# Kernel optimization log

Hardware: AMD Instinct MI355X
Metric: run time of the kernel (lower is better)

## Reference

```python
import jax, jax.numpy as jnp
import numpy as np
from jax import lax

EPS = 1e-5
DN_CONV = ('NCDHW', 'OIDHW', 'NCDHW')
DN_TCONV = ('NCDHW', 'DHWIO', 'NCDHW')


def conv3(x, w, s):
    # 3x3x3 conv, padding 1 (dense analogue of sparse conv on the voxel grid)
    return lax.conv_general_dilated(x, w, (s, s, s), [(1, 1)] * 3, dimension_numbers=DN_CONV)


def tconv3(x, w, s):
    # 3x3x3 transposed conv; stride 2 doubles spatial size, stride 1 keeps it
    return lax.conv_transpose(x, w, (s, s, s), 'SAME', dimension_numbers=DN_TCONV)


def bn_relu(x, g, b):
    # BatchNorm over (N,D,H,W) per channel, training-mode batch stats, then ReLU
    m = jnp.mean(x, (0, 2, 3, 4), keepdims=True)
    v = jnp.var(x, (0, 2, 3, 4), keepdims=True)
    y = (x - m) * lax.rsqrt(v + EPS) * g[None, :, None, None, None] + b[None, :, None, None, None]
    return jax.nn.relu(y)


def setup_inputs() -> dict:
    key = jax.random.key(0)
    ks = jax.random.split(key, 8)
    W = lambda k, shape: jax.random.normal(k, shape, dtype=jnp.float32) * 0.05
    inp = {
        'x': jax.random.normal(ks[0], (2, 16, 64, 64, 64), dtype=jnp.float32),
        # encoder convs (OIDHW)
        'w0': W(ks[1], (32, 16, 3, 3, 3)), 'g0': jnp.ones((32,)), 'b0': jnp.zeros((32,)),
        'w1': W(ks[2], (64, 32, 3, 3, 3)), 'g1': jnp.ones((64,)), 'b1': jnp.zeros((64,)),
        'w2': W(ks[3], (128, 64, 3, 3, 3)), 'g2': jnp.ones((128,)), 'b2': jnp.zeros((128,)),
        # reconstruction decoder transposed convs (DHWIO)
        'wt2r': W(ks[4], (3, 3, 3, 128, 64)), 'g2r': jnp.ones((64,)), 'b2r': jnp.zeros((64,)),
        'wt1r': W(ks[5], (3, 3, 3, 64, 32)), 'g1r': jnp.ones((32,)), 'b1r': jnp.zeros((32,)),
        'wt0r': W(jax.random.fold_in(key, 10), (3, 3, 3, 32, 16)),
        # classification decoder transposed convs
        'wt2c': W(ks[6], (3, 3, 3, 128, 64)), 'g2c': jnp.ones((64,)), 'b2c': jnp.zeros((64,)),
        'wt1c': W(ks[7], (3, 3, 3, 128, 64)), 'g1c': jnp.ones((64,)), 'b1c': jnp.zeros((64,)),
        'wt0c': W(jax.random.fold_in(key, 11), (3, 3, 3, 96, 2)),
    }
    return inp


def reference(x, w0, g0, b0, w1, g1, b1, w2, g2, b2,
              wt2r, g2r, b2r, wt1r, g1r, b1r, wt0r,
              wt2c, g2c, b2c, wt1c, g1c, b1c, wt0c):
    # encoder
    s1 = bn_relu(conv3(x, w0, 1), g0, b0)      # [N,32,64,64,64]
    s2 = bn_relu(conv3(s1, w1, 2), g1, b1)     # [N,64,32,32,32]
    s4 = bn_relu(conv3(s2, w2, 2), g2, b2)     # [N,128,16,16,16]
    # reconstruction head
    rec = bn_relu(tconv3(s4, wt2r, 2), g2r, b2r)  # [N,64,32,...]
    # classification head with skip concats
    cl = bn_relu(tconv3(s4, wt2c, 2), g2c, b2c)   # [N,64,32,...]
    cl = jnp.concatenate([cl, s2], axis=1)        # [N,128,32,...]
    rec = bn_relu(tconv3(rec, wt1r, 2), g1r, b1r)  # [N,32,64,...]
    cl = bn_relu(tconv3(cl, wt1c, 2), g1c, b1c)    # [N,64,64,...]
    cl = jnp.concatenate([cl, s1], axis=1)         # [N,96,64,...]
    rec = tconv3(rec, wt0r, 1)                     # [N,16,64,...]
    cl = tconv3(cl, wt0c, 1)                       # [N,2,64,...]
    return (cl, rec)
```

## Files before the change

kernel.cpp:

```cpp
#include <hip/hip_runtime.h>
#include <hip/hip_bf16.h>


using bf16 = __hip_bfloat16;
using ushort4v = __attribute__((ext_vector_type(4))) unsigned short;
using ushort8  = __attribute__((ext_vector_type(8))) unsigned short;
using short8   = __attribute__((ext_vector_type(8))) short;
using f32x4    = __attribute__((ext_vector_type(4))) float;
using float4v  = __attribute__((ext_vector_type(4))) float;

#define TPB 256

static inline int cdiv_l(long a, int b){ return (int)((a + b - 1) / b); }

__device__ __forceinline__ float b2f(unsigned short u){
  union { unsigned int i; float f; } v; v.i = ((unsigned int)u) << 16; return v.f;
}
__device__ __forceinline__ unsigned short f2b(float f){
  union { bf16 h; unsigned short u; } v; v.h = __float2bfloat16(f); return v.u;
}
__device__ __forceinline__ ushort8 bnApply8(ushort8 v, const float* sc, const float* sh, int c){
  float4v s0 = *(const float4v*)(sc + c), s1v = *(const float4v*)(sc + c + 4);
  float4v h0 = *(const float4v*)(sh + c), h1v = *(const float4v*)(sh + c + 4);
  ushort8 r;
#pragma unroll
  for (int j = 0; j < 4; ++j){ float y = b2f(v[j]) * s0[j] + h0[j]; r[j] = f2b(y > 0.f ? y : 0.f); }
#pragma unroll
  for (int j = 0; j < 4; ++j){ float y = b2f(v[j+4]) * s1v[j] + h1v[j]; r[j+4] = f2b(y > 0.f ? y : 0.f); }
  return r;
}

__global__ void rp_all(const float* __restrict__ w0, const float* __restrict__ w1,
                       const float* __restrict__ w2, const float* __restrict__ wt2r,
                       const float* __restrict__ wt2c, const float* __restrict__ wt1r,
                       const float* __restrict__ wt1c, const float* __restrict__ wt0r,
                       const float* __restrict__ wt0c,
                       unsigned short* __restrict__ wb0p, unsigned short* __restrict__ wb1,
                       unsigned short* __restrict__ wb2, unsigned short* __restrict__ wb2r,
                       unsigned short* __restrict__ wb2c, unsigned short* __restrict__ wb1r,
                       unsigned short* __restrict__ wb1c, unsigned short* __restrict__ wbrec,
                       unsigned short* __restrict__ wbcl){
  int idx = blockIdx.x * TPB + threadIdx.x;
  auto enc = [](const float* w, unsigned short* d, int i, int Cin, int Cout){
    int ci = i % Cin; int t = i / Cin; int co = t % Cout; int tap = t / Cout;
    d[i] = f2b(w[((long)co * Cin + ci) * 27 + tap]);
  };
  auto dec = [](const float* w, unsigned short* d, int i, int Cin, int Cout, int CIP, int COP){
    int ci = i % CIP; int t = i / CIP; int co = t % COP; int tap = t / COP;
    float v = (ci < Cin && co < Cout) ? w[((long)tap * Cin + ci) * Cout + co] : 0.f;
    d[i] = f2b(v);
  };
  if (idx < 14336) {
    int i = idx;
    int k = i & 31; int t = i >> 5; int co = t & 31; int pp = t >> 5;
    int tap = pp * 2 + (k >> 4); int ci = k & 15;
    float v = (tap < 27) ? w0[((long)co * 16 + ci) * 27 + tap] : 0.f;
    wb0p[i] = f2b(v);
  }
  else if (idx <   69632) enc(w1,  wb1,  idx - 14336,  32, 64);
  else if (idx <  290816) enc(w2,  wb2,  idx - 69632,  64, 128);
  else if (idx <  512000) dec(wt2r, wb2r, idx - 290816, 128, 64, 128, 64);
  else if (idx <  733184) dec(wt2c, wb2c, idx - 512000, 128, 64, 128, 64);
  else if (idx <  788480) dec(wt1r, wb1r, idx - 733184,  64, 32,  64, 32);
  else if (idx < 1009664) dec(wt1c, wb1c, idx - 788480, 128, 64, 128, 64);
  else if (idx < 1023488) dec(wt0r, wbrec, idx - 1009664, 32, 16,  32, 16);
  else if (idx < 1064960) dec(wt0c, wbcl, idx - 1023488, 96,  2,  96, 16);
}

__global__ void xpose_k(const float* __restrict__ x, unsigned short* __restrict__ xt){
  __shared__ float l[16][257];
  int t = threadIdx.x;
  long p0 = (long)blockIdx.x * 256;
  int n = (int)(p0 >> 18);
  long off = p0 & 262143;
  const float* xb = x + ((long)n * 16) * 262144 + off;
#pragma unroll
  for (int c = 0; c < 16; ++c) l[c][t] = xb[(long)c * 262144 + t];
  __syncthreads();
  ushort8 u0, u1;
#pragma unroll
  for (int k = 0; k < 8; ++k){ u0[k] = f2b(l[k][t]); u1[k] = f2b(l[k + 8][t]); }
  unsigned short* o = xt + (p0 + t) * 16;
  *(ushort8*)o = u0; *(ushort8*)(o + 8) = u1;
}

template <int CO_TILES, bool STATS>
__global__ __launch_bounds__(TPB, 2) void tconv_quad(
    const unsigned short* __restrict__ inA, int CA,
    const unsigned short* __restrict__ inB, int CB,
    const float* __restrict__ scA, const float* __restrict__ shA,
    const unsigned short* __restrict__ wb,
    unsigned short* __restrict__ out,
    float* __restrict__ part2, int NB,
    int N, int Cout, int COP, int CIP, int G) {
  __shared__ unsigned short xs[2][4 * 432 * 8];
  const int tid = threadIdx.x, wv = tid >> 6, l = tid & 63, l15 = l & 15, lg = l >> 4;
  int ntW = G >> 4, ntH = G >> 2, ntD = G >> 2;
  int bx = blockIdx.x;
  const int blkLin = blockIdx.x * 4 + blockIdx.z;
  int w0 = (bx % ntW) << 4; bx /= ntW;
  int h0 = (bx % ntH) << 2; bx /= ntH;
  int d0 = (bx % ntD) << 2; int n = bx / ntD;
  const int co0 = blockIdx.y * (16 * CO_TILES);
  const int quad = blockIdx.z;
  const int pd = (quad >> 1) & 1, ph = quad & 1;
  const long spin = (long)G * G * G;

  int nkd, kd_[2], dd_[2], nkh, kh_[2], dh_[2];
  if (pd){ nkd=1; kd_[0]=1; dd_[0]=0; } else { nkd=2; kd_[0]=0; dd_[0]=-1; kd_[1]=2; dd_[1]=0; }
  if (ph){ nkh=1; kh_[0]=1; dh_[0]=0; } else { nkh=2; kh_[0]=0; dh_[0]=-1; kh_[1]=2; dh_[1]=0; }

  f32x4 acc[CO_TILES][4][2];
#pragma unroll
  for (int ct = 0; ct < CO_TILES; ++ct)
#pragma unroll
    for (int j = 0; j < 4; ++j)
#pragma unroll
      for (int p = 0; p < 2; ++p) acc[ct][j][p] = (f32x4){0.f, 0.f, 0.f, 0.f};

  auto stage = [&](int ch, int buf) {
    int c0 = ch << 5;
    const unsigned short* src; int Cs, cl_; bool useBN;
    if (c0 < CA){ src = inA; Cs = CA; cl_ = c0; useBN = (scA != nullptr); }
    else        { src = inB; Cs = CB; cl_ = c0 - CA; useBN = false; }
    const unsigned short* sb = src + (long)n * Cs * spin;
    unsigned short* xb = &xs[buf][0];
    for (int idx = tid; idx < 4 * 425; idx += TPB) {
      int q = idx / 425, pt = idx - q * 425;
      int zw = pt % 17; int zt = pt / 17; int zh = zt % 5; int zd = zt / 5;
      int gd = d0 + zd - 1, gh = h0 + zh - 1, gw = w0 + zw - 1;
      ushort8 v = (ushort8){0,0,0,0,0,0,0,0};
      if ((unsigned)gd < (unsigned)G && (unsigned)gh < (unsigned)G && (unsigned)gw < (unsigned)G) {
        v = *(const ushort8*)(sb + (((long)gd * G + gh) * G + gw) * Cs + cl_ + q * 8);
        if (useBN) v = bnApply8(v, scA, shA, cl_ + q * 8);
      }
      *(ushort8*)(xb + (q * 432 + pt) * 8) = v;
    }
  };

  const int nch = CIP >> 5;
  stage(0, 0);
  __syncthreads();
#pragma unroll 1
  for (int ch = 0; ch < nch; ++ch) {
    int cur = ch & 1;
    int c0 = ch << 5;
    if (ch + 1 < nch) stage(ch + 1, cur ^ 1);
    const unsigned short* xr = &xs[cur][0];
#pragma unroll 1
    for (int a = 0; a < nkd; ++a) {
      int zd = wv + 1 + dd_[a];
#pragma unroll 1
      for (int b = 0; b < nkh; ++b) {
        int tapb = (kd_[a] * 3 + kh_[b]) * 3;
        const unsigned short* ap = wb + ((long)tapb * COP + co0 + l15) * CIP + c0 + lg * 8;
        long tstride = (long)COP * CIP;
        short8 Ak0[CO_TILES], Ak1[CO_TILES], Ak2[CO_TILES];
#pragma unroll
        for (int ct = 0; ct < CO_TILES; ++ct) {
          Ak0[ct] = *(const short8*)(ap + ct * 16 * CIP);
          Ak1[ct] = *(const short8*)(ap + tstride + ct * 16 * CIP);
          Ak2[ct] = *(const short8*)(ap + 2 * tstride + ct * 16 * CIP);
        }
        int zh0 = 1 + dh_[b];
#pragma unroll
        for (int j = 0; j < 4; ++j) {
          int basept = (zd * 5 + (j + zh0)) * 17 + l15;
          short8 Bm = *(const short8*)(xr + (lg * 432 + basept) * 8);
          short8 B0 = *(const short8*)(xr + (lg * 432 + basept + 1) * 8);
#pragma unroll
          for (int ct = 0; ct < CO_TILES; ++ct) {
            acc[ct][j][0] = __builtin_amdgcn_mfma_f32_16x16x32_bf16(Ak0[ct], Bm, acc[ct][j][0], 0, 0, 0);
            acc[ct][j][0] = __builtin_amdgcn_mfma_f32_16x16x32_bf16(Ak2[ct], B0, acc[ct][j][0], 0, 0, 0);
            acc[ct][j][1] = __builtin_amdgcn_mfma_f32_16x16x32_bf16(Ak1[ct], B0, acc[ct][j][1], 0, 0, 0);
          }
        }
      }
    }
    __syncthreads();
  }

  int Gout = 2 * G; long spo = (long)Gout * Gout * Gout;
  int od = 2 * (d0 + wv) + pd;
#pragma unroll
  for (int j = 0; j < 4; ++j) {
    int oh = 2 * (h0 + j) + ph;
#pragma unroll
    for (int p = 0; p < 2; ++p) {
      int ow = 2 * (w0 + l15) + p;
      long pt = ((long)od * Gout + oh) * Gout + ow;
#pragma unroll
      for (int ct = 0; ct < CO_TILES; ++ct) {
        ushort4v pk;
#pragma unroll
        for (int r = 0; r < 4; ++r) pk[r] = f2b(acc[ct][j][p][r]);
        *(ushort4v*)(out + ((long)n * spo + pt) * Cout + co0 + ct * 16 + lg * 4) = pk;
      }
    }
  }

  if constexpr (STATS) {
    __shared__ float redS[4][CO_TILES][4][4];
    __shared__ float redQ[4][CO_TILES][4][4];
#pragma unroll
    for (int ct = 0; ct < CO_TILES; ++ct)
#pragma unroll
      for (int r = 0; r < 4; ++r) {
        float s = 0.f, q = 0.f;
#pragma unroll
        for (int j = 0; j < 4; ++j)
#pragma unroll
          for (int p = 0; p < 2; ++p) { float a = acc[ct][j][p][r]; s += a; q += a * a; }
#pragma unroll
        for (int m = 1; m < 16; m <<= 1) { s += __shfl_xor(s, m); q += __shfl_xor(q, m); }
        if (l15 == 0) { redS[wv][ct][lg][r] = s; redQ[wv][ct][lg][r] = q; }
      }
    __syncthreads();
    if (tid < CO_TILES * 16) {
      int ct = tid >> 4, lg2 = (tid >> 2) & 3, r = tid & 3;
      float s = 0.f, q = 0.f;
#pragma unroll
      for (int w2 = 0; w2 < 4; ++w2) { s += redS[w2][ct][lg2][r]; q += redQ[w2][ct][lg2][r]; }
      int c = co0 + ct * 16 + lg2 * 4 + r;
      long slot = (long)c * NB + blkLin;
      part2[slot * 2] = s; part2[slot * 2 + 1] = q;
    }
  }
}

__global__ __launch_bounds__(TPB) void tconv_dual(
    const unsigned short* __restrict__ in, int CI,
    const float* __restrict__ scA, const float* __restrict__ shA,
    const unsigned short* __restrict__ wbA, const unsigned short* __restrict__ wbB,
    unsigned short* __restrict__ outA, unsigned short* __restrict__ outB,
    float* __restrict__ p2A, float* __restrict__ p2B, int NB,
    int N, int Cout, int COP, int CIP, int G) {
  const int CT = 2;
  __shared__ unsigned short xs[4 * 432 * 8];
  const int tid = threadIdx.x, wv = tid >> 6, l = tid & 63, l15 = l & 15, lg = l >> 4;
  int ntW = G >> 4, ntH = G >> 2, ntD = G >> 2;
  int bx = blockIdx.x;
  const int blkLin = blockIdx.x * 4 + blockIdx.z;
  int w0 = (bx % ntW) << 4; bx /= ntW;
  int h0 = (bx % ntH) << 2; bx /= ntH;
  int d0 = (bx % ntD) << 2; int n = bx / ntD;
  const int co0 = blockIdx.y * (16 * CT);
  const int quad = blockIdx.z;
  const int pd = (quad >> 1) & 1, ph = quad & 1;
  const long spin = (long)G * G * G;

  int nkd, kd_[2], dd_[2], nkh, kh_[2], dh_[2];
  if (pd){ nkd=1; kd_[0]=1; dd_[0]=0; } else { nkd=2; kd_[0]=0; dd_[0]=-1; kd_[1]=2; dd_[1]=0; }
  if (ph){ nkh=1; kh_[0]=1; dh_[0]=0; } else { nkh=2; kh_[0]=0; dh_[0]=-1; kh_[1]=2; dh_[1]=0; }

  f32x4 acc[2][CT][4][2];
#pragma unroll
  for (int h = 0; h < 2; ++h)
#pragma unroll
    for (int ct = 0; ct < CT; ++ct)
#pragma unroll
      for (int j = 0; j < 4; ++j)
#pragma unroll
        for (int p = 0; p < 2; ++p) acc[h][ct][j][p] = (f32x4){0.f, 0.f, 0.f, 0.f};

  const int nch = CIP >> 5;
#pragma unroll 1
  for (int ch = 0; ch < nch; ++ch) {
    int c0 = ch << 5;
    const unsigned short* sb = in + (long)n * CI * spin;
    __syncthreads();
    for (int idx = tid; idx < 4 * 425; idx += TPB) {
      int q = idx / 425, pt = idx - q * 425;
      int zw = pt % 17; int zt = pt / 17; int zh = zt % 5; int zd = zt / 5;
      int gd = d0 + zd - 1, gh = h0 + zh - 1, gw = w0 + zw - 1;
      ushort8 v = (ushort8){0,0,0,0,0,0,0,0};
      if ((unsigned)gd < (unsigned)G && (unsigned)gh < (unsigned)G && (unsigned)gw < (unsigned)G) {
        v = *(const ushort8*)(sb + (((long)gd * G + gh) * G + gw) * CI + c0 + q * 8);
        v = bnApply8(v, scA, shA, c0 + q * 8);
      }
      *(ushort8*)(xs + (q * 432 + pt) * 8) = v;
    }
    __syncthreads();
#pragma unroll 1
    for (int a = 0; a < nkd; ++a) {
      int zd = wv + 1 + dd_[a];
#pragma unroll 1
      for (int b = 0; b < nkh; ++b) {
        int tapb = (kd_[a] * 3 + kh_[b]) * 3;
        long tstride = (long)COP * CIP;
        long abase = ((long)tapb * COP + co0 + l15) * CIP + c0 + lg * 8;
        int zh0 = 1 + dh_[b];
#pragma unroll
        for (int h = 0; h < 2; ++h) {
          const unsigned short* ap = (h == 0 ? wbA : wbB) + abase;
          short8 Ak0[CT], Ak1[CT], Ak2[CT];
#pragma unroll
          for (int ct = 0; ct < CT; ++ct) {
            Ak0[ct] = *(const short8*)(ap + ct * 16 * CIP);
            Ak1[ct] = *(const short8*)(ap + tstride + ct * 16 * CIP);
            Ak2[ct] = *(const short8*)(ap + 2 * tstride + ct * 16 * CIP);
          }
#pragma unroll
          for (int j = 0; j < 4; ++j) {
            int basept = (zd * 5 + (j + zh0)) * 17 + l15;
            short8 Bm = *(const short8*)(xs + (lg * 432 + basept) * 8);
            short8 B0 = *(const short8*)(xs + (lg * 432 + basept + 1) * 8);
#pragma unroll
            for (int ct = 0; ct < CT; ++ct) {
              acc[h][ct][j][0] = __builtin_amdgcn_mfma_f32_16x16x32_bf16(Ak0[ct], Bm, acc[h][ct][j][0], 0, 0, 0);
              acc[h][ct][j][0] = __builtin_amdgcn_mfma_f32_16x16x32_bf16(Ak2[ct], B0, acc[h][ct][j][0], 0, 0, 0);
              acc[h][ct][j][1] = __builtin_amdgcn_mfma_f32_16x16x32_bf16(Ak1[ct], B0, acc[h][ct][j][1], 0, 0, 0);
            }
          }
        }
      }
    }
  }

  int Gout = 2 * G; long spo = (long)Gout * Gout * Gout;
  int od = 2 * (d0 + wv) + pd;
#pragma unroll
  for (int j = 0; j < 4; ++j) {
    int oh = 2 * (h0 + j) + ph;
#pragma unroll
    for (int p = 0; p < 2; ++p) {
      int ow = 2 * (w0 + l15) + p;
      long pt = ((long)od * Gout + oh) * Gout + ow;
#pragma unroll
      for (int h = 0; h < 2; ++h) {
        unsigned short* o = h == 0 ? outA : outB;
#pragma unroll
        for (int ct = 0; ct < CT; ++ct) {
          ushort4v pk;
#pragma unroll
          for (int r = 0; r < 4; ++r) pk[r] = f2b(acc[h][ct][j][p][r]);
          *(ushort4v*)(o + ((long)n * spo + pt) * Cout + co0 + ct * 16 + lg * 4) = pk;
        }
      }
    }
  }

  __shared__ float redS[4][CT][4][4];
  __shared__ float redQ[4][CT][4][4];
#pragma unroll 1
  for (int h = 0; h < 2; ++h) {
    __syncthreads();
#pragma unroll
    for (int ct = 0; ct < CT; ++ct)
#pragma unroll
      for (int r = 0; r < 4; ++r) {
        float s = 0.f, q = 0.f;
#pragma unroll
        for (int j = 0; j < 4; ++j)
#pragma unroll
          for (int p = 0; p < 2; ++p) { float a = acc[h][ct][j][p][r]; s += a; q += a * a; }
#pragma unroll
        for (int m = 1; m < 16; m <<= 1) { s += __shfl_xor(s, m); q += __shfl_xor(q, m); }
        if (l15 == 0) { redS[wv][ct][lg][r] = s; redQ[wv][ct][lg][r] = q; }
      }
    __syncthreads();
    if (tid < CT * 16) {
      int ct = tid >> 4, lg2 = (tid >> 2) & 3, r = tid & 3;
      float s = 0.f, q = 0.f;
#pragma unroll
      for (int w2 = 0; w2 < 4; ++w2) { s += redS[w2][ct][lg2][r]; q += redQ[w2][ct][lg2][r]; }
      int c = co0 + ct * 16 + lg2 * 4 + r;
      long slot = (long)c * NB + blkLin;
      float* p2 = h == 0 ? p2A : p2B;
      p2[slot * 2] = s; p2[slot * 2 + 1] = q;
    }
  }
}

template <int VARIANT, int CO_TILES, bool PAIRED, bool FOUT, bool STATS>
__global__ __launch_bounds__(TPB) void mconv(
    const unsigned short* __restrict__ inA, int CA,
    const unsigned short* __restrict__ inB, int CB,
    const float* __restrict__ scA, const float* __restrict__ shA,
    const unsigned short* __restrict__ wb,
    void* __restrict__ outv,
    float* __restrict__ part2, int NB,
    int N, int Cout, int COP, int CIP, int G) {
  const int tid = threadIdx.x, wv = tid >> 6, l = tid & 63, l15 = l & 15, lg = l >> 4;
  int bx = blockIdx.x;
  const int blkLin = blockIdx.x;
  int w0, h0, d0, n;
  int wvd = wv & 1, jh = wv >> 1, jbase = jh * 4;
  if constexpr (VARIANT == 0) {
    int ntW = G >> 4, ntH = G >> 3, ntD = G >> 1;
    w0 = (bx % ntW) << 4; bx /= ntW;
    h0 = (bx % ntH) << 3; bx /= ntH;
    d0 = (bx % ntD) << 1; n = bx / ntD;
  } else {
    int ntW = G >> 4, ntH = G >> 2, ntD = G >> 2;
    w0 = (bx % ntW) << 4; bx /= ntW;
    h0 = (bx % ntH) << 2; bx /= ntH;
    d0 = (bx % ntD) << 2; n = bx / ntD;
  }
  const int co0 = blockIdx.y * (16 * CO_TILES);
  const int Gin = (VARIANT == 2) ? 2 * G : G;
  const long spin = (long)Gin * Gin * Gin;

  f32x4 acc[CO_TILES][4];
#pragma unroll
  for (int ct = 0; ct < CO_TILES; ++ct)
#pragma unroll
    for (int j = 0; j < 4; ++j) acc[ct][j] = (f32x4){0.f, 0.f, 0.f, 0.f};

  if constexpr (PAIRED) {
    __shared__ unsigned short xs[2 * 728 * 8];
    const unsigned short* src = inA + (long)n * 16 * spin;
    for (int idx = tid; idx < 2 * 720; idx += TPB) {
      int q = idx / 720, pt = idx - q * 720;
      int zw = pt % 18; int zt = pt / 18; int zh = zt % 10; int zd = zt / 10;
      int gd = d0 + zd - 1, gh = h0 + zh - 1, gw = w0 + zw - 1;
      ushort8 v = (ushort8){0,0,0,0,0,0,0,0};
      if ((unsigned)gd < (unsigned)G && (unsigned)gh < (unsigned)G && (unsigned)gw < (unsigned)G)
        v = *(const ushort8*)(src + (((long)gd * G + gh) * G + gw) * 16 + q * 8);
      *(ushort8*)(xs + (q * 728 + pt) * 8) = v;
    }
    __syncthreads();
#pragma unroll 1
    for (int pp = 0; pp < 14; ++pp) {
      short8 A0 = *(const short8*)(wb + ((pp * 32 + l15) * 32) + lg * 8);
      short8 A1 = *(const short8*)(wb + ((pp * 32 + 16 + l15) * 32) + lg * 8);
      int t0 = 2 * pp + (lg >> 1); if (t0 > 26) t0 = 26;
      int dd = t0 / 9 - 1, dh = (t0 / 3) % 3 - 1, dw = t0 % 3 - 1;
      int q = lg & 1;
      int zd = wvd + 1 + dd;
      int base = (q * 728 + (zd * 10 + (1 + dh + jbase)) * 18 + 1 + l15 + dw) * 8;
#pragma unroll
      for (int j = 0; j < 4; ++j) {
        short8 B = *(const short8*)(xs + base + j * (18 * 8));
        acc[0][j] = __builtin_amdgcn_mfma_f32_16x16x32_bf16(A0, B, acc[0][j], 0, 0, 0);
        if (CO_TILES == 2)
          acc[1][j] = __builtin_amdgcn_mfma_f32_16x16x32_bf16(A1, B, acc[1][j], 0, 0, 0);
      }
    }
  } else if constexpr (VARIANT == 0) {
    __shared__ unsigned short xs[4 * 728 * 8];
    const int nch = CIP >> 5;
#pragma unroll 1
    for (int ch = 0; ch < nch; ++ch) {
      int c0 = ch << 5;
      const unsigned short* src; int Cs, cl_; bool useBN;
      if (c0 < CA){ src = inA; Cs = CA; cl_ = c0; useBN = (scA != nullptr); }
      else        { src = inB; Cs = CB; cl_ = c0 - CA; useBN = false; }
      const unsigned short* sb = src + (long)n * Cs * spin;
      __syncthreads();
      for (int idx = tid; idx < 4 * 720; idx += TPB) {
        int q = idx / 720, pt = idx - q * 720;
        int zw = pt % 18; int zt = pt / 18; int zh = zt % 10; int zd = zt / 10;
        int gd = d0 + zd - 1, gh = h0 + zh - 1, gw = w0 + zw - 1;
        ushort8 v = (ushort8){0,0,0,0,0,0,0,0};
        if ((unsigned)gd < (unsigned)G && (unsigned)gh < (unsigned)G && (unsigned)gw < (unsigned)G) {
          v = *(const ushort8*)(sb + (((long)gd * G + gh) * G + gw) * Cs + cl_ + q * 8);
          if (useBN) v = bnApply8(v, scA, shA, cl_ + q * 8);
        }
        *(ushort8*)(xs + (q * 728 + pt) * 8) = v;
      }
      __syncthreads();
#pragma unroll 1
      for (int a = 0; a < 3; ++a) {
        int zd = wvd + a;
        short8 A0[3][3], A1[3][3];
#pragma unroll
        for (int b = 0; b < 3; ++b)
#pragma unroll
          for (int c = 0; c < 3; ++c) {
            int tap = (a * 3 + b) * 3 + c;
            const unsigned short* ap = wb + ((long)tap * COP + co0 + l15) * CIP + c0 + lg * 8;
            A0[b][c] = *(const short8*)ap;
            if (CO_TILES == 2) A1[b][c] = *(const short8*)(ap + 16 * CIP);
          }
#pragma unroll
        for (int sl = 0; sl < 6; ++sl) {
          int sg = jbase + sl;
          int rb = (lg * 728 + (zd * 10 + sg) * 18 + l15) * 8;
          short8 B0 = *(const short8*)(xs + rb);
          short8 B1 = *(const short8*)(xs + rb + 8);
          short8 B2 = *(const short8*)(xs + rb + 16);
#pragma unroll
          for (int b = 0; b < 3; ++b) {
            int j = sl - b;
            if (j >= 0 && j < 4) {
              acc[0][j] = __builtin_amdgcn_mfma_f32_16x16x32_bf16(A0[b][0], B0, acc[0][j], 0, 0, 0);
              acc[0][j] = __builtin_amdgcn_mfma_f32_16x16x32_bf16(A0[b][1], B1, acc[0][j], 0, 0, 0);
              acc[0][j] = __builtin_amdgcn_mfma_f32_16x16x32_bf16(A0[b][2], B2, acc[0][j], 0, 0, 0);
              if (CO_TILES == 2) {
                acc[1][j] = __builtin_amdgcn_mfma_f32_16x16x32_bf16(A1[b][0], B0, acc[1][j], 0, 0, 0);
                acc[1][j] = __builtin_amdgcn_mfma_f32_16x16x32_bf16(A1[b][1], B1, acc[1][j], 0, 0, 0);
                acc[1][j] = __builtin_amdgcn_mfma_f32_16x16x32_bf16(A1[b][2], B2, acc[1][j], 0, 0, 0);
              }
            }
          }
        }
      }
    }
  } else {
    const int nch = CIP >> 5;
#pragma unroll 1
    for (int ch = 0; ch < nch; ++ch) {
      int c0 = ch << 5;
      const unsigned short* src; int Cs, cl_;
      if (c0 < CA){ src = inA; Cs = CA; cl_ = c0; } else { src = inB; Cs = CB; cl_ = c0 - CA; }
      const unsigned short* sb = src + (long)n * Cs * spin;
#pragma unroll 1
      for (int a = 0; a < 3; ++a) {
        int gd = 2 * (d0 + wv) + a - 1;
        bool vd = (unsigned)gd < (unsigned)Gin;
#pragma unroll 1
        for (int b = 0; b < 3; ++b) {
#pragma unroll
          for (int c = 0; c < 3; ++c) {
            int tap = (a * 3 + b) * 3 + c;
            const unsigned short* ap = wb + ((long)tap * COP + co0 + l15) * CIP + c0 + lg * 8;
            short8 A0 = *(const short8*)ap;
            short8 A1;
            if (CO_TILES == 2) A1 = *(const short8*)(ap + 16 * CIP);
            int gw = 2 * (w0 + l15) + c - 1;
            bool vdw = vd && ((unsigned)gw < (unsigned)Gin);
#pragma unroll
            for (int j = 0; j < 4; ++j) {
              int gh = 2 * (h0 + j) + b - 1;
              short8 B = (short8){0,0,0,0,0,0,0,0};
              if (vdw && (unsigned)gh < (unsigned)Gin)
                B = *(const short8*)(sb + (((long)gd * Gin + gh) * Gin + gw) * Cs + cl_ + lg * 8);
              acc[0][j] = __builtin_amdgcn_mfma_f32_16x16x32_bf16(A0, B, acc[0][j], 0, 0, 0);
              if (CO_TILES == 2)
                acc[1][j] = __builtin_amdgcn_mfma_f32_16x16x32_bf16(A1, B, acc[1][j], 0, 0, 0);
            }
          }
        }
      }
    }
  }

  const long spo = (long)G * G * G;
#pragma unroll
  for (int j = 0; j < 4; ++j) {
    long pt;
    if constexpr (VARIANT == 0)
      pt = ((long)(d0 + wvd) * G + (h0 + jbase + j)) * G + (w0 + l15);
    else
      pt = ((long)(d0 + wv) * G + (h0 + j)) * G + (w0 + l15);
    if constexpr (!FOUT) {
      unsigned short* outp = (unsigned short*)outv;
#pragma unroll
      for (int ct = 0; ct < CO_TILES; ++ct) {
        ushort4v pk;
#pragma unroll
        for (int r = 0; r < 4; ++r) pk[r] = f2b(acc[ct][j][r]);
        *(ushort4v*)(outp + ((long)n * spo + pt) * Cout + co0 + ct * 16 + lg * 4) = pk;
      }
    } else {
      float* outp = (float*)outv;
#pragma unroll
      for (int ct = 0; ct < CO_TILES; ++ct)
#pragma unroll
        for (int r = 0; r < 4; ++r) {
          int co = co0 + ct * 16 + lg * 4 + r;
          if (co < Cout) outp[((long)(n * Cout + co)) * spo + pt] = acc[ct][j][r];
        }
    }
  }

  if constexpr (STATS) {
    __shared__ float redS[4][CO_TILES][4][4];
    __shared__ float redQ[4][CO_TILES][4][4];
#pragma unroll
    for (int ct = 0; ct < CO_TILES; ++ct)
#pragma unroll
      for (int r = 0; r < 4; ++r) {
        float s = 0.f, q = 0.f;
#pragma unroll
        for (int j = 0; j < 4; ++j) { float a = acc[ct][j][r]; s += a; q += a * a; }
#pragma unroll
        for (int m = 1; m < 16; m <<= 1) { s += __shfl_xor(s, m); q += __shfl_xor(q, m); }
        if (l15 == 0) { redS[wv][ct][lg][r] = s; redQ[wv][ct][lg][r] = q; }
      }
    __syncthreads();
    if (tid < CO_TILES * 16) {
      int ct = tid >> 4, lg2 = (tid >> 2) & 3, r = tid & 3;
      float s = 0.f, q = 0.f;
#pragma unroll
      for (int w2 = 0; w2 < 4; ++w2) { s += redS[w2][ct][lg2][r]; q += redQ[w2][ct][lg2][r]; }
      int c = co0 + ct * 16 + lg2 * 4 + r;
      long slot = (long)c * NB + blkLin;
      part2[slot * 2] = s; part2[slot * 2 + 1] = q;
    }
  }
}

__global__ void bn_stats2b(const float* __restrict__ part2, const float* __restrict__ g,
                           const float* __restrict__ b, float* __restrict__ sc,
                           float* __restrict__ sh, int NB, float inv_cnt){
  int c = blockIdx.x, tid = threadIdx.x;
  float s = 0.f, q = 0.f;
  for (int i = tid; i < NB; i += TPB) {
    s += part2[((long)c * NB + i) * 2];
    q += part2[((long)c * NB + i) * 2 + 1];
  }
  __shared__ float ss[TPB], qq[TPB];
  ss[tid] = s; qq[tid] = q;
  __syncthreads();
  for (int off = TPB / 2; off > 0; off >>= 1) {
    if (tid < off) { ss[tid] += ss[tid + off]; qq[tid] += qq[tid + off]; }
    __syncthreads();
  }
  if (tid == 0) {
    float m = ss[0] * inv_cnt, v = qq[0] * inv_cnt - m * m;
    float rs = rsqrtf(v + 1e-5f) * g[c];
    sc[c] = rs;
    sh[c] = b[c] - m * rs;
  }
}

__global__ void bn_relu_cl(unsigned short* __restrict__ x, const float* __restrict__ sc,
                           const float* __restrict__ sh, int C, long tot8){
  long i8 = (long)blockIdx.x * TPB + threadIdx.x;
  if (i8 >= tot8) return;
  long e = i8 * 8;
  int c0 = (int)(e & (C - 1));
  ushort8 v = *(ushort8*)(x + e);
  *(ushort8*)(x + e) = bnApply8(v, sc, sh, c0);
}

extern "C" void kernel_launch(void* const* d_in, const int* in_sizes, int n_in,
                              void* d_out, int out_size, void* d_ws, size_t ws_size,
                              hipStream_t stream) {
  const float* x    = (const float*)d_in[0];
  const float* w0   = (const float*)d_in[1];
  const float* g0   = (const float*)d_in[2];
  const float* b0   = (const float*)d_in[3];
  const float* w1   = (const float*)d_in[4];
  const float* g1   = (const float*)d_in[5];
  const float* b1   = (const float*)d_in[6];
  const float* w2   = (const float*)d_in[7];
  const float* g2   = (const float*)d_in[8];
  const float* b2   = (const float*)d_in[9];
  const float* wt2r = (const float*)d_in[10];
  const float* g2r  = (const float*)d_in[11];
  const float* b2r  = (const float*)d_in[12];
  const float* wt1r = (const float*)d_in[13];
  const float* g1r  = (const float*)d_in[14];
  const float* b1r  = (const float*)d_in[15];
  const float* wt0r = (const float*)d_in[16];
  const float* wt2c = (const float*)d_in[17];
  const float* g2c  = (const float*)d_in[18];
  const float* b2c  = (const float*)d_in[19];
  const float* wt1c = (const float*)d_in[20];
  const float* g1c  = (const float*)d_in[21];
  const float* b1c  = (const float*)d_in[22];
  const float* wt0c = (const float*)d_in[23];

  const int N = 2;
  const long sp64 = 262144, sp32 = 32768, sp16 = 4096;

  unsigned short* W = (unsigned short*)d_ws;
  unsigned short* s1   = W;
  unsigned short* s2   = s1  + 16777216;
  unsigned short* s4   = s2  + 4194304;
  unsigned short* r32  = s4  + 1048576;
  unsigned short* c32  = r32 + 4194304;
  unsigned short* r64  = c32 + 4194304;
  unsigned short* xt   = r64;
  unsigned short* c64  = r64 + 16777216;
  unsigned short* wb0p = c64 + 33554432;
  unsigned short* wb1  = wb0p + 14336;
  unsigned short* wb2  = wb1  + 55296;
  unsigned short* wb2r = wb2  + 221184;
  unsigned short* wb2c = wb2r + 221184;
  unsigned short* wb1r = wb2c + 221184;
  unsigned short* wb1c = wb1r + 55296;
  unsigned short* wbrec= wb1c + 221184;
  unsigned short* wbcl = wbrec+ 13824;
  float* part2  = (float*)(wbcl + 41472);
  float* part2b = part2 + 131072;
  float* bsc  = part2b + 16384;
  float* bsh  = bsc + 128;
  float* sc_s4  = bsh  + 128; float* sh_s4  = sc_s4  + 128;
  float* sc_r32 = sh_s4 + 128; float* sh_r32 = sc_r32 + 128;
  float* sc_c32 = sh_r32+ 128; float* sh_c32 = sc_c32 + 128;
  float* sc_r64 = sh_c32+ 128; float* sh_r64 = sc_r64 + 128;
  float* sc_c64 = sh_r64+ 128; float* sh_c64 = sc_c64 + 128;

  float* out_cl  = (float*)d_out;
  float* out_rec = (float*)d_out + 2L * 2 * sp64;

  rp_all<<<cdiv_l(1064960, TPB), TPB, 0, stream>>>(
      w0, w1, w2, wt2r, wt2c, wt1r, wt1c, wt0r, wt0c,
      wb0p, wb1, wb2, wb2r, wb2c, wb1r, wb1c, wbrec, wbcl);
  xpose_k<<<2048, TPB, 0, stream>>>(x, xt);

  auto gx0 = [&](int G){ return (unsigned)(N * (G >> 1) * (G >> 3) * (G >> 4)); };
  auto gx  = [&](int G){ return (unsigned)(N * (G >> 2) * (G >> 2) * (G >> 4)); };

  mconv<0, 2, true, false, true><<<dim3(gx0(64), 1), TPB, 0, stream>>>(
      xt, 16, nullptr, 0, nullptr, nullptr, wb0p, s1, part2, (int)gx0(64), N, 32, 32, 32, 64);
  bn_stats2b<<<32, TPB, 0, stream>>>(part2, g0, b0, bsc, bsh, (int)gx0(64), 1.f / (float)(2 * sp64));
  bn_relu_cl<<<cdiv_l(2 * sp64 * 32 / 8, TPB), TPB, 0, stream>>>(s1, bsc, bsh, 32, 2 * sp64 * 32 / 8);

  mconv<2, 2, false, false, true><<<dim3(gx(32), 2), TPB, 0, stream>>>(
      s1, 32, nullptr, 0, nullptr, nullptr, wb1, s2, part2, (int)gx(32), N, 64, 64, 32, 32);
  bn_stats2b<<<64, TPB, 0, stream>>>(part2, g1, b1, bsc, bsh, (int)gx(32), 1.f / (float)(2 * sp32));
  bn_relu_cl<<<cdiv_l(2 * sp32 * 64 / 8, TPB), TPB, 0, stream>>>(s2, bsc, bsh, 64, 2 * sp32 * 64 / 8);

  mconv<2, 1, false, false, true><<<dim3(gx(16), 8), TPB, 0, stream>>>(
      s2, 64, nullptr, 0, nullptr, nullptr, wb2, s4, part2, (int)gx(16), N, 128, 128, 64, 16);
  bn_stats2b<<<128, TPB, 0, stream>>>(part2, g2, b2, sc_s4, sh_s4, (int)gx(16), 1.f / (float)(2 * sp16));

  tconv_dual<<<dim3(gx(16), 2, 4), TPB, 0, stream>>>(
      s4, 128, sc_s4, sh_s4, wb2r, wb2c, r32, c32, part2, part2b, (int)gx(16) * 4,
      N, 64, 64, 128, 16);
  bn_stats2b<<<64, TPB, 0, stream>>>(part2, g2r, b2r, sc_r32, sh_r32, (int)gx(16) * 4, 1.f / (float)(2 * sp32));
  bn_stats2b<<<64, TPB, 0, stream>>>(part2b, g2c, b2c, sc_c32, sh_c32, (int)gx(16) * 4, 1.f / (float)(2 * sp32));

  tconv_quad<2, true><<<dim3(gx(32), 1, 4), TPB, 0, stream>>>(
      r32, 64, nullptr, 0, sc_r32, sh_r32, wb1r, r64, part2, (int)gx(32) * 4, N, 32, 32, 64, 32);
  bn_stats2b<<<32, TPB, 0, stream>>>(part2, g1r, b1r, sc_r64, sh_r64, (int)gx(32) * 4, 1.f / (float)(2 * sp64));
  tconv_quad<4, true><<<dim3(gx(32), 1, 4), TPB, 0, stream>>>(
      c32, 64, s2, 64, sc_c32, sh_c32, wb1c, c64, part2, (int)gx(32) * 4, N, 64, 64, 128, 32);
  bn_stats2b<<<64, TPB, 0, stream>>>(part2, g1c, b1c, sc_c64, sh_c64, (int)gx(32) * 4, 1.f / (float)(2 * sp64));

  mconv<0, 1, false, true, false><<<dim3(gx0(64), 1), TPB, 0, stream>>>(
      r64, 32, nullptr, 0, sc_r64, sh_r64, wbrec, out_rec, nullptr, 0, N, 16, 16, 32, 64);
  mconv<0, 1, false, true, false><<<dim3(gx0(64), 1), TPB, 0, stream>>>(
      c64, 64, s1, 32, sc_c64, sh_c64, wbcl, out_cl, nullptr, 0, N, 2, 16, 96, 64);
}
```

Measured before the change: 567.3 us.

## Fuse encoder BN+ReLU into consumer conv loads, drop bn_relu_cl passes

```diff
diff --git a/kernel.cpp b/kernel.cpp
--- a/kernel.cpp
+++ b/kernel.cpp
@@ -18,6 +18,9 @@
 }
 __device__ __forceinline__ unsigned short f2b(float f){
   union { bf16 h; unsigned short u; } v; v.h = __float2bfloat16(f); return v.u;
+}
+__device__ __forceinline__ short8 asS8(ushort8 u){
+  union { ushort8 a; short8 b; } x; x.a = u; return x.b;
 }
 __device__ __forceinline__ ushort8 bnApply8(ushort8 v, const float* sc, const float* sh, int c){
   float4v s0 = *(const float4v*)(sc + c), s1v = *(const float4v*)(sc + c + 4);
@@ -89,6 +92,7 @@
     const unsigned short* __restrict__ inA, int CA,
     const unsigned short* __restrict__ inB, int CB,
     const float* __restrict__ scA, const float* __restrict__ shA,
+    const float* __restrict__ scB, const float* __restrict__ shB,
     const unsigned short* __restrict__ wb,
     unsigned short* __restrict__ out,
     float* __restrict__ part2, int NB,
@@ -120,9 +124,10 @@
 
   auto stage = [&](int ch, int buf) {
     int c0 = ch << 5;
-    const unsigned short* src; int Cs, cl_; bool useBN;
-    if (c0 < CA){ src = inA; Cs = CA; cl_ = c0; useBN = (scA != nullptr); }
-    else        { src = inB; Cs = CB; cl_ = c0 - CA; useBN = false; }
+    const unsigned short* src; int Cs, cl_;
+    const float* scU; const float* shU;
+    if (c0 < CA){ src = inA; Cs = CA; cl_ = c0; scU = scA; shU = shA; }
+    else        { src = inB; Cs = CB; cl_ = c0 - CA; scU = scB; shU = shB; }
     const unsigned short* sb = src + (long)n * Cs * spin;
     unsigned short* xb = &xs[buf][0];
     for (int idx = tid; idx < 4 * 425; idx += TPB) {
@@ -132,7 +137,7 @@
       ushort8 v = (ushort8){0,0,0,0,0,0,0,0};
       if ((unsigned)gd < (unsigned)G && (unsigned)gh < (unsigned)G && (unsigned)gw < (unsigned)G) {
         v = *(const ushort8*)(sb + (((long)gd * G + gh) * G + gw) * Cs + cl_ + q * 8);
-        if (useBN) v = bnApply8(v, scA, shA, cl_ + q * 8);
+        if (scU) v = bnApply8(v, scU, shU, cl_ + q * 8);
       }
       *(ushort8*)(xb + (q * 432 + pt) * 8) = v;
     }
@@ -377,6 +382,7 @@
     const unsigned short* __restrict__ inA, int CA,
     const unsigned short* __restrict__ inB, int CB,
     const float* __restrict__ scA, const float* __restrict__ shA,
+    const float* __restrict__ scB, const float* __restrict__ shB,
     const unsigned short* __restrict__ wb,
     void* __restrict__ outv,
     float* __restrict__ part2, int NB,
@@ -443,9 +449,10 @@
 #pragma unroll 1
     for (int ch = 0; ch < nch; ++ch) {
       int c0 = ch << 5;
-      const unsigned short* src; int Cs, cl_; bool useBN;
-      if (c0 < CA){ src = inA; Cs = CA; cl_ = c0; useBN = (scA != nullptr); }
-      else        { src = inB; Cs = CB; cl_ = c0 - CA; useBN = false; }
+      const unsigned short* src; int Cs, cl_;
+      const float* scU; const float* shU;
+      if (c0 < CA){ src = inA; Cs = CA; cl_ = c0; scU = scA; shU = shA; }
+      else        { src = inB; Cs = CB; cl_ = c0 - CA; scU = scB; shU = shB; }
       const unsigned short* sb = src + (long)n * Cs * spin;
       __syncthreads();
       for (int idx = tid; idx < 4 * 720; idx += TPB) {
@@ -455,7 +462,7 @@
         ushort8 v = (ushort8){0,0,0,0,0,0,0,0};
         if ((unsigned)gd < (unsigned)G && (unsigned)gh < (unsigned)G && (unsigned)gw < (unsigned)G) {
           v = *(const ushort8*)(sb + (((long)gd * G + gh) * G + gw) * Cs + cl_ + q * 8);
-          if (useBN) v = bnApply8(v, scA, shA, cl_ + q * 8);
+          if (scU) v = bnApply8(v, scU, shU, cl_ + q * 8);
         }
         *(ushort8*)(xs + (q * 728 + pt) * 8) = v;
       }
@@ -503,7 +510,9 @@
     for (int ch = 0; ch < nch; ++ch) {
       int c0 = ch << 5;
       const unsigned short* src; int Cs, cl_;
-      if (c0 < CA){ src = inA; Cs = CA; cl_ = c0; } else { src = inB; Cs = CB; cl_ = c0 - CA; }
+      const float* scU; const float* shU;
+      if (c0 < CA){ src = inA; Cs = CA; cl_ = c0; scU = scA; shU = shA; }
+      else        { src = inB; Cs = CB; cl_ = c0 - CA; scU = scB; shU = shB; }
       const unsigned short* sb = src + (long)n * Cs * spin;
 #pragma unroll 1
       for (int a = 0; a < 3; ++a) {
@@ -524,8 +533,11 @@
             for (int j = 0; j < 4; ++j) {
               int gh = 2 * (h0 + j) + b - 1;
               short8 B = (short8){0,0,0,0,0,0,0,0};
-              if (vdw && (unsigned)gh < (unsigned)Gin)
-                B = *(const short8*)(sb + (((long)gd * Gin + gh) * Gin + gw) * Cs + cl_ + lg * 8);
+              if (vdw && (unsigned)gh < (unsigned)Gin) {
+                ushort8 u = *(const ushort8*)(sb + (((long)gd * Gin + gh) * Gin + gw) * Cs + cl_ + lg * 8);
+                if (scU) u = bnApply8(u, scU, shU, cl_ + lg * 8);
+                B = asS8(u);
+              }
               acc[0][j] = __builtin_amdgcn_mfma_f32_16x16x32_bf16(A0, B, acc[0][j], 0, 0, 0);
               if (CO_TILES == 2)
                 acc[1][j] = __builtin_amdgcn_mfma_f32_16x16x32_bf16(A1, B, acc[1][j], 0, 0, 0);
@@ -614,16 +626,6 @@
     sc[c] = rs;
     sh[c] = b[c] - m * rs;
   }
-}
-
-__global__ void bn_relu_cl(unsigned short* __restrict__ x, const float* __restrict__ sc,
-                           const float* __restrict__ sh, int C, long tot8){
-  long i8 = (long)blockIdx.x * TPB + threadIdx.x;
-  if (i8 >= tot8) return;
-  long e = i8 * 8;
-  int c0 = (int)(e & (C - 1));
-  ushort8 v = *(ushort8*)(x + e);
-  *(ushort8*)(x + e) = bnApply8(v, sc, sh, c0);
 }
 
 extern "C" void kernel_launch(void* const* d_in, const int* in_sizes, int n_in,
@@ -677,13 +679,13 @@
   unsigned short* wbcl = wbrec+ 13824;
   float* part2  = (float*)(wbcl + 41472);
   float* part2b = part2 + 131072;
-  float* bsc  = part2b + 16384;
-  float* bsh  = bsc + 128;
-  float* sc_s4  = bsh  + 128; float* sh_s4  = sc_s4  + 128;
-  float* sc_r32 = sh_s4 + 128; float* sh_r32 = sc_r32 + 128;
-  float* sc_c32 = sh_r32+ 128; float* sh_c32 = sc_c32 + 128;
-  float* sc_r64 = sh_c32+ 128; float* sh_r64 = sc_r64 + 128;
-  float* sc_c64 = sh_r64+ 128; float* sh_c64 = sc_c64 + 128;
+  float* sc_s1  = part2b + 16384; float* sh_s1  = sc_s1 + 128;
+  float* sc_s2  = sh_s1 + 128;    float* sh_s2  = sc_s2 + 128;
+  float* sc_s4  = sh_s2 + 128;    float* sh_s4  = sc_s4 + 128;
+  float* sc_r32 = sh_s4 + 128;    float* sh_r32 = sc_r32 + 128;
+  float* sc_c32 = sh_r32 + 128;   float* sh_c32 = sc_c32 + 128;
+  float* sc_r64 = sh_c32 + 128;   float* sh_r64 = sc_r64 + 128;
+  float* sc_c64 = sh_r64 + 128;   float* sh_c64 = sc_c64 + 128;
 
   float* out_cl  = (float*)d_out;
   float* out_rec = (float*)d_out + 2L * 2 * sp64;
@@ -697,17 +699,18 @@
   auto gx  = [&](int G){ return (unsigned)(N * (G >> 2) * (G >> 2) * (G >> 4)); };
 
   mconv<0, 2, true, false, true><<<dim3(gx0(64), 1), TPB, 0, stream>>>(
-      xt, 16, nullptr, 0, nullptr, nullptr, wb0p, s1, part2, (int)gx0(64), N, 32, 32, 32, 64);
-  bn_stats2b<<<32, TPB, 0, stream>>>(part2, g0, b0, bsc, bsh, (int)gx0(64), 1.f / (float)(2 * sp64));
-  bn_relu_cl<<<cdiv_l(2 * sp64 * 32 / 8, TPB), TPB, 0, stream>>>(s1, bsc, bsh, 32, 2 * sp64 * 32 / 8);
+      xt, 16, nullptr, 0, nullptr, nullptr, nullptr, nullptr, wb0p, s1,
+      part2, (int)gx0(64), N, 32, 32, 32, 64);
+  bn_stats2b<<<32, TPB, 0, stream>>>(part2, g0, b0, sc_s1, sh_s1, (int)gx0(64), 1.f / (float)(2 * sp64));
 
   mconv<2, 2, false, false, true><<<dim3(gx(32), 2), TPB, 0, stream>>>(
-      s1, 32, nullptr, 0, nullptr, nullptr, wb1, s2, part2, (int)gx(32), N, 64, 64, 32, 32);
-  bn_stats2b<<<64, TPB, 0, stream>>>(part2, g1, b1, bsc, bsh, (int)gx(32), 1.f / (float)(2 * sp32));
-  bn_relu_cl<<<cdiv_l(2 * sp32 * 64 / 8, TPB), TPB, 0, stream>>>(s2, bsc, bsh, 64, 2 * sp32 * 64 / 8);
+      s1, 32, nullptr, 0, sc_s1, sh_s1, nullptr, nullptr, wb1, s2,
+      part2, (int)gx(32), N, 64, 64, 32, 32);
+  bn_stats2b<<<64, TPB, 0, stream>>>(part2, g1, b1, sc_s2, sh_s2, (int)gx(32), 1.f / (float)(2 * sp32));
 
   mconv<2, 1, false, false, true><<<dim3(gx(16), 8), TPB, 0, stream>>>(
-      s2, 64, nullptr, 0, nullptr, nullptr, wb2, s4, part2, (int)gx(16), N, 128, 128, 64, 16);
+      s2, 64, nullptr, 0, sc_s2, sh_s2, nullptr, nullptr, wb2, s4,
+      part2, (int)gx(16), N, 128, 128, 64, 16);
   bn_stats2b<<<128, TPB, 0, stream>>>(part2, g2, b2, sc_s4, sh_s4, (int)gx(16), 1.f / (float)(2 * sp16));
 
   tconv_dual<<<dim3(gx(16), 2, 4), TPB, 0, stream>>>(
@@ -717,14 +720,18 @@
   bn_stats2b<<<64, TPB, 0, stream>>>(part2b, g2c, b2c, sc_c32, sh_c32, (int)gx(16) * 4, 1.f / (float)(2 * sp32));
 
   tconv_quad<2, true><<<dim3(gx(32), 1, 4), TPB, 0, stream>>>(
-      r32, 64, nullptr, 0, sc_r32, sh_r32, wb1r, r64, part2, (int)gx(32) * 4, N, 32, 32, 64, 32);
+      r32, 64, nullptr, 0, sc_r32, sh_r32, nullptr, nullptr, wb1r, r64,
+      part2, (int)gx(32) * 4, N, 32, 32, 64, 32);
   bn_stats2b<<<32, TPB, 0, stream>>>(part2, g1r, b1r, sc_r64, sh_r64, (int)gx(32) * 4, 1.f / (float)(2 * sp64));
   tconv_quad<4, true><<<dim3(gx(32), 1, 4), TPB, 0, stream>>>(
-      c32, 64, s2, 64, sc_c32, sh_c32, wb1c, c64, part2, (int)gx(32) * 4, N, 64, 64, 128, 32);
+      c32, 64, s2, 64, sc_c32, sh_c32, sc_s2, sh_s2, wb1c, c64,
+      part2, (int)gx(32) * 4, N, 64, 64, 128, 32);
   bn_stats2b<<<64, TPB, 0, stream>>>(part2, g1c, b1c, sc_c64, sh_c64, (int)gx(32) * 4, 1.f / (float)(2 * sp64));
 
   mconv<0, 1, false, true, false><<<dim3(gx0(64), 1), TPB, 0, stream>>>(
-      r64, 32, nullptr, 0, sc_r64, sh_r64, wbrec, out_rec, nullptr, 0, N, 16, 16, 32, 64);
+      r64, 32, nullptr, 0, sc_r64, sh_r64, nullptr, nullptr, wbrec, out_rec,
+      nullptr, 0, N, 16, 16, 32, 64);
   mconv<0, 1, false, true, false><<<dim3(gx0(64), 1), TPB, 0, stream>>>(
-      c64, 64, s1, 32, sc_c64, sh_c64, wbcl, out_cl, nullptr, 0, N, 2, 16, 96, 64);
-}
+      c64, 64, s1, 32, sc_c64, sh_c64, sc_s1, sh_s1, wbcl, out_cl,
+      nullptr, 0, N, 2, 16, 96, 64);
+}
```

Result: slower. 601.0 us (+6.0%).
